# Kernel optimization log

Hardware: AMD Instinct MI355X
Metric: run time of the kernel (lower is better)

## Reference

```python
import jax, jax.numpy as jnp
import numpy as np

EMBED_DIM = 1024
N_HEADS = 16
HEAD_DIM = EMBED_DIM // N_HEADS


def setup_inputs() -> dict:
    key = jax.random.key(0)
    k_x, k_qw, k_qb, k_ow, k_ob = jax.random.split(key, 5)
    s = 1.0 / np.sqrt(EMBED_DIM)
    return {
        "x": jax.random.normal(k_x, (2, 2048, EMBED_DIM), dtype=jnp.float32),
        "qkv_w": jax.random.uniform(k_qw, (3 * EMBED_DIM, EMBED_DIM), jnp.float32, -s, s),
        "qkv_b": jax.random.uniform(k_qb, (3 * EMBED_DIM,), jnp.float32, -s, s),
        "out_w": jax.random.uniform(k_ow, (EMBED_DIM, EMBED_DIM), jnp.float32, -s, s),
        "out_b": jax.random.uniform(k_ob, (EMBED_DIM,), jnp.float32, -s, s),
    }


def reference(x, qkv_w, qkv_b, out_w, out_b):
    B, S, E = x.shape
    # fused QKV projection (torch Linear: x @ W^T + b)
    qkv = x @ qkv_w.T + qkv_b                      # [B,S,3E]
    qkv = qkv.reshape(B, S, N_HEADS, 3 * HEAD_DIM).transpose(0, 2, 1, 3)  # [B,H,S,3d]
    q, k, v = jnp.split(qkv, 3, axis=-1)           # each [B,H,S,d]
    scores = jnp.einsum("bhqd,bhkd->bhqk", q, k) / jnp.sqrt(jnp.float32(HEAD_DIM))
    weights = jax.nn.softmax(scores, axis=-1)      # [B,H,S,S]
    attn = jnp.einsum("bhqk,bhkd->bhqd", weights, v)
    attn = attn.transpose(0, 2, 1, 3).reshape(B, S, E)
    return attn @ out_w.T + out_b
```

## Files before the change

### kernel.cpp

```cpp
#include <hip/hip_runtime.h>
#include <hip/hip_bf16.h>


#define E_DIM   1024
#define NHEADS  16
#define HDIM    64
#define SEQ     2048
#define TOK     4096
#define QKV_DIM 3072
#define QK_STRIDE 2048
#define QSCALE_F 0.18033688011112042f

typedef __attribute__((ext_vector_type(8))) short bf16x8;
typedef __attribute__((ext_vector_type(4))) float f32x4;
typedef __attribute__((ext_vector_type(4))) int   i32x4;
typedef __attribute__((ext_vector_type(2))) int   i32x2;
typedef __attribute__((ext_vector_type(2))) __bf16 bf16x2_t;

__device__ __forceinline__ unsigned short f2bf(float x) {
    union { float f; unsigned u; } a; a.f = x;
    unsigned r = a.u + 0x7FFF + ((a.u >> 16) & 1);
    return (unsigned short)(r >> 16);
}

__device__ __forceinline__ unsigned pack2bf(float a, float b) {
#if __has_builtin(__builtin_amdgcn_cvt_pk_bf16_f32)
    union { bf16x2_t v; unsigned u; } u;
    u.v = __builtin_amdgcn_cvt_pk_bf16_f32(a, b);
    return u.u;
#else
    union { float f; unsigned u; } ua, ub; ua.f = a; ub.f = b;
    unsigned ra = ua.u + 0x7FFF + ((ua.u >> 16) & 1);
    unsigned rb = ub.u + 0x7FFF + ((ub.u >> 16) & 1);
    return (ra >> 16) | (rb & 0xFFFF0000u);
#endif
}

__device__ __forceinline__ void load_lds16(const void* g, void* l) {
    __builtin_amdgcn_global_load_lds(
        (const __attribute__((address_space(1))) void*)g,
        (__attribute__((address_space(3))) void*)l, 16, 0, 0);
}

__device__ __forceinline__ bf16x8 lds_read8(const unsigned short* p) {
    union { i32x4 i; bf16x8 b; } u;
    u.i = *(const i32x4*)p;
    return u.b;
}

__device__ __forceinline__ f32x4 mfma16(bf16x8 a, bf16x8 b, f32x4 c) {
    return __builtin_amdgcn_mfma_f32_16x16x32_bf16(a, b, c, 0, 0, 0);
}

__global__ void cast3_kernel(const float* __restrict__ a, unsigned short* __restrict__ oa, int na4,
                             const float* __restrict__ b, unsigned short* __restrict__ ob, int nb4,
                             const float* __restrict__ c, unsigned short* __restrict__ oc) {
    int i = blockIdx.x * blockDim.x + threadIdx.x;
    const float* src; unsigned short* dst; int j;
    if (i < na4)            { src = a; dst = oa; j = i; }
    else if (i < na4 + nb4) { src = b; dst = ob; j = i - na4; }
    else                    { src = c; dst = oc; j = i - na4 - nb4; }
    f32x4 v = ((const f32x4*)src)[j];
    union { i32x2 i2; unsigned u[2]; } o;
    o.u[0] = pack2bf(v.x, v.y);
    o.u[1] = pack2bf(v.z, v.w);
    ((i32x2*)dst)[j] = o.i2;
}

__global__ __launch_bounds__(256, 3)
void gemm_qkv_kernel(const unsigned short* __restrict__ A,
                     const unsigned short* __restrict__ B,
                     const float* __restrict__ bias,
                     unsigned short* __restrict__ qk,
                     unsigned short* __restrict__ vT,
                     int K) {
    __shared__ __align__(16) unsigned short As[128 * 64];
    __shared__ __align__(16) unsigned short Bs[128 * 64];

    const int tid  = threadIdx.x;
    const int wave = tid >> 6, lane = tid & 63;
    const int quad = lane >> 4, l16 = lane & 15;
    const int row0 = blockIdx.y * 128, col0 = blockIdx.x * 128;
    const int wr = (wave >> 1) * 64, wc = (wave & 1) * 64;

    f32x4 acc[4][4];
#pragma unroll
    for (int i = 0; i < 4; ++i)
#pragma unroll
        for (int j = 0; j < 4; ++j) acc[i][j] = (f32x4){0.f, 0.f, 0.f, 0.f};

    const int nkt = K >> 6;
    for (int kt = 0; kt < nkt; ++kt) {
        const int k0 = kt << 6;
#pragma unroll
        for (int i = 0; i < 4; ++i) {
            int p = i * 256 + tid;
            int r = p >> 3;
            int kc = (p & 7) ^ (r & 7);
            load_lds16(A + (size_t)(row0 + r) * K + k0 + kc * 8, &As[p * 8]);
        }
#pragma unroll
        for (int i = 0; i < 4; ++i) {
            int p = i * 256 + tid;
            int r = p >> 3;
            int kc = (p & 7) ^ (r & 7);
            load_lds16(B + (size_t)(col0 + r) * K + k0 + kc * 8, &Bs[p * 8]);
        }
        __syncthreads();

#pragma unroll
        for (int ks = 0; ks < 2; ++ks) {
            bf16x8 af[4], bfr[4];
#pragma unroll
            for (int rb = 0; rb < 4; ++rb) {
                int r_l  = wr + rb * 16 + l16;
                int phys = (ks * 4 + quad) ^ (l16 & 7);
                af[rb] = lds_read8(&As[r_l * 64 + phys * 8]);
            }
#pragma unroll
            for (int cb = 0; cb < 4; ++cb) {
                int r_l  = wc + cb * 16 + l16;
                int phys = (ks * 4 + quad) ^ (l16 & 7);
                bfr[cb] = lds_read8(&Bs[r_l * 64 + phys * 8]);
            }
#pragma unroll
            for (int rb = 0; rb < 4; ++rb)
#pragma unroll
                for (int cb = 0; cb < 4; ++cb)
                    acc[rb][cb] = mfma16(af[rb], bfr[cb], acc[rb][cb]);
        }
        __syncthreads();
    }

#pragma unroll
    for (int rb = 0; rb < 4; ++rb)
#pragma unroll
        for (int cb = 0; cb < 4; ++cb) {
            int col = col0 + wc + cb * 16 + l16;
            int h    = col / 192;
            int part = col - h * 192;
            float bv = bias[col];
            int row_b = row0 + wr + rb * 16 + quad * 4;
            float v[4];
#pragma unroll
            for (int reg = 0; reg < 4; ++reg) v[reg] = acc[rb][cb][reg] + bv;
            if (part < 128) {
                float sc = (part < 64) ? QSCALE_F : 1.0f;
                size_t base = (size_t)h * 128 + part;
#pragma unroll
                for (int reg = 0; reg < 4; ++reg)
                    qk[(size_t)(row_b + reg) * QK_STRIDE + base] = f2bf(v[reg] * sc);
            } else {
                int i  = part - 128;
                int b  = row_b >> 11;
                int s  = row_b & 2047;
                i32x2 pk;
                pk.x = (int)pack2bf(v[0], v[1]);
                pk.y = (int)pack2bf(v[2], v[3]);
                *(i32x2*)&vT[(((size_t)(b * 16 + h)) * 64 + i) * SEQ + s] = pk;
            }
        }
}

__global__ __launch_bounds__(256, 2)
void gemm2_kernel(const unsigned short* __restrict__ A,
                  const unsigned short* __restrict__ B,
                  const float* __restrict__ bias,
                  float* __restrict__ C, int M, int N, int K) {
    __shared__ __align__(16) unsigned short As[128 * 64];
    __shared__ __align__(16) unsigned short Bs[64 * 64];

    const int tid  = threadIdx.x;
    const int wave = tid >> 6, lane = tid & 63;
    const int quad = lane >> 4, l16 = lane & 15;
    const int row0 = blockIdx.y * 128, col0 = blockIdx.x * 64;
    const int wr = wave * 32;

    f32x4 acc[2][4];
#pragma unroll
    for (int i = 0; i < 2; ++i)
#pragma unroll
        for (int j = 0; j < 4; ++j) acc[i][j] = (f32x4){0.f, 0.f, 0.f, 0.f};

    const int nkt = K >> 6;
    for (int kt = 0; kt < nkt; ++kt) {
        const int k0 = kt << 6;
#pragma unroll
        for (int i = 0; i < 4; ++i) {
            int p = i * 256 + tid;
            int r = p >> 3;
            int kc = (p & 7) ^ (r & 7);
            load_lds16(A + (size_t)(row0 + r) * K + k0 + kc * 8, &As[p * 8]);
        }
#pragma unroll
        for (int i = 0; i < 2; ++i) {
            int p = i * 256 + tid;
            int r = p >> 3;
            int kc = (p & 7) ^ (r & 7);
            load_lds16(B + (size_t)(col0 + r) * K + k0 + kc * 8, &Bs[p * 8]);
        }
        __syncthreads();

#pragma unroll
        for (int ks = 0; ks < 2; ++ks) {
            bf16x8 af[2], bfr[4];
#pragma unroll
            for (int rb = 0; rb < 2; ++rb) {
                int r_l  = wr + rb * 16 + l16;
                int phys = (ks * 4 + quad) ^ (l16 & 7);
                af[rb] = lds_read8(&As[r_l * 64 + phys * 8]);
            }
#pragma unroll
            for (int cb = 0; cb < 4; ++cb) {
                int r_l  = cb * 16 + l16;
                int phys = (ks * 4 + quad) ^ (l16 & 7);
                bfr[cb] = lds_read8(&Bs[r_l * 64 + phys * 8]);
            }
#pragma unroll
            for (int rb = 0; rb < 2; ++rb)
#pragma unroll
                for (int cb = 0; cb < 4; ++cb)
                    acc[rb][cb] = mfma16(af[rb], bfr[cb], acc[rb][cb]);
        }
        __syncthreads();
    }

#pragma unroll
    for (int rb = 0; rb < 2; ++rb)
#pragma unroll
        for (int cb = 0; cb < 4; ++cb) {
            int col = col0 + cb * 16 + l16;
            float bv = bias[col];
#pragma unroll
            for (int reg = 0; reg < 4; ++reg) {
                int row = row0 + wr + rb * 16 + quad * 4 + reg;
                C[(size_t)row * N + col] = acc[rb][cb][reg] + bv;
            }
        }
}

__global__ __launch_bounds__(256, 4)
void attn_kernel(const unsigned short* __restrict__ qk,
                 const unsigned short* __restrict__ vT,
                 unsigned short* __restrict__ attn) {
    __shared__ __align__(16) unsigned short Ks[128 * 64];
    __shared__ __align__(16) unsigned short Vs[64 * 128];
    __shared__ __align__(16) unsigned short Ps[4][16 * 64];

    const int tid  = threadIdx.x;
    const int wave = tid >> 6, lane = tid & 63;
    const int quad = lane >> 4, l16 = lane & 15;
    const int bh = blockIdx.y;
    const int b = bh >> 4, h = bh & 15;
    const int q0 = blockIdx.x * 64;
    const size_t rowbase = (size_t)b * SEQ;
    const int qtok = q0 + wave * 16 + l16;

    bf16x8 qf[2];
#pragma unroll
    for (int ks = 0; ks < 2; ++ks) {
        const unsigned short* p =
            qk + (rowbase + qtok) * QK_STRIDE + h * 128 + ks * 32 + quad * 8;
        union { i32x4 i; bf16x8 b; } u;
        u.i = *(const i32x4*)p;
        qf[ks] = u.b;
    }

    f32x4 o[4];
#pragma unroll
    for (int ib = 0; ib < 4; ++ib) o[ib] = (f32x4){0.f, 0.f, 0.f, 0.f};
    float l_s = 0.f;

    for (int kt = 0; kt < SEQ / 128; ++kt) {
        const int kb = kt * 128;
        const unsigned short* kbase = qk + (rowbase + kb) * QK_STRIDE + h * 128 + 64;
        const unsigned short* vbase = vT + (size_t)bh * 64 * SEQ + kb;
#pragma unroll
        for (int i = 0; i < 4; ++i) {
            int p = i * 256 + tid;
            int r = p >> 3;
            int kc = (p & 7) ^ (r & 7);
            load_lds16(kbase + r * QK_STRIDE + kc * 8, &Ks[p * 8]);
        }
#pragma unroll
        for (int i = 0; i < 4; ++i) {
            int p = i * 256 + tid;
            int r = p >> 4;
            int c = (p & 15) ^ (r & 15);
            load_lds16(vbase + r * SEQ + c * 8, &Vs[p * 8]);
        }
        __syncthreads();

        f32x4 s[8];
#pragma unroll
        for (int cb = 0; cb < 8; ++cb) s[cb] = (f32x4){0.f, 0.f, 0.f, 0.f};
#pragma unroll
        for (int ks = 0; ks < 2; ++ks)
#pragma unroll
            for (int cb = 0; cb < 8; ++cb) {
                int phys = (ks * 4 + quad) ^ (l16 & 7);
                bf16x8 kf = lds_read8(&Ks[(cb * 16 + l16) * 64 + phys * 8]);
                s[cb] = mfma16(kf, qf[ks], s[cb]);
            }

        float rs = 0.f;
#pragma unroll
        for (int cb = 0; cb < 8; ++cb)
#pragma unroll
            for (int r = 0; r < 4; ++r) {
                float pv = exp2f(s[cb][r]);
                s[cb][r] = pv;
                rs += pv;
            }
        rs += __shfl_xor(rs, 16);
        rs += __shfl_xor(rs, 32);
        l_s += rs;

#pragma unroll
        for (int half = 0; half < 2; ++half) {
#pragma unroll
            for (int c4 = 0; c4 < 4; ++c4) {
                int cb = half * 4 + c4;
                i32x2 pk;
                pk.x = (int)pack2bf(s[cb][0], s[cb][1]);
                pk.y = (int)pack2bf(s[cb][2], s[cb][3]);
                int off = l16 * 64 + (((c4 * 2 + (quad >> 1)) ^ (l16 & 7)) * 8)
                        + (quad & 1) * 4;
                *(i32x2*)&Ps[wave][off] = pk;
            }
            __asm__ volatile("s_waitcnt lgkmcnt(0)" ::: "memory");
#pragma unroll
            for (int kc2 = 0; kc2 < 2; ++kc2) {
                bf16x8 pf = lds_read8(
                    &Ps[wave][l16 * 64 + (((kc2 * 4 + quad) ^ (l16 & 7)) * 8)]);
#pragma unroll
                for (int ib = 0; ib < 4; ++ib) {
                    int hk = half * 2 + kc2;
                    int phys = (hk * 4 + quad) ^ l16;
                    bf16x8 vf = lds_read8(&Vs[(ib * 16 + l16) * 128 + phys * 8]);
                    o[ib] = mfma16(pf, vf, o[ib]);
                }
            }
        }
        __syncthreads();
    }

    float il[4];
#pragma unroll
    for (int r = 0; r < 4; ++r) il[r] = 1.0f / __shfl(l_s, quad * 4 + r);
#pragma unroll
    for (int ib = 0; ib < 4; ++ib)
#pragma unroll
        for (int r = 0; r < 4; ++r) {
            int t = q0 + wave * 16 + quad * 4 + r;
            attn[(rowbase + t) * E_DIM + h * 64 + ib * 16 + l16] =
                f2bf(o[ib][r] * il[r]);
        }
}

extern "C" void kernel_launch(void* const* d_in, const int* in_sizes, int n_in,
                              void* d_out, int out_size, void* d_ws, size_t ws_size,
                              hipStream_t stream) {
    const float* x     = (const float*)d_in[0];
    const float* qkv_w = (const float*)d_in[1];
    const float* qkv_b = (const float*)d_in[2];
    const float* out_w = (const float*)d_in[3];
    const float* out_b = (const float*)d_in[4];

    char* ws = (char*)d_ws;
    unsigned short* xb   = (unsigned short*)(ws);
    unsigned short* wqkv = (unsigned short*)(ws + 8388608);
    unsigned short* wout = (unsigned short*)(ws + 14680064);
    unsigned short* qk   = (unsigned short*)(ws + 16777216);
    unsigned short* attn = (unsigned short*)(ws + 33554432);
    unsigned short* vT   = (unsigned short*)(ws + 41943040);

    cast3_kernel<<<8192, 256, 0, stream>>>(x, xb, 1048576,
                                           qkv_w, wqkv, 786432,
                                           out_w, wout);

    gemm_qkv_kernel<<<dim3(24, 32), 256, 0, stream>>>(
        xb, wqkv, qkv_b, qk, vT, E_DIM);

    attn_kernel<<<dim3(32, 32), 256, 0, stream>>>(qk, vT, attn);

    gemm2_kernel<<<dim3(16, 32), 256, 0, stream>>>(
        attn, wout, out_b, (float*)d_out, TOK, E_DIM, E_DIM);
}
```

Measured before the change: 207.7 us.

## Double attention block to 128 queries with 8 waves sharing K/V tiles

The attention kernel now runs 512 threads per block covering 128 query rows, so each K/V tile staged in LDS serves twice as many queries and the total global K/V traffic is halved. LDS addresses are precomputed as per-lane base pointers to cut index arithmetic inside the loop. exp2f is swapped for the hardware exp2 builtin, and f2bf now uses the packed conversion. The risks are fewer blocks in the grid (512 instead of 1024) and higher register pressure under the new launch bounds.

```diff
diff --git a/kernel.cpp b/kernel.cpp
--- a/kernel.cpp
+++ b/kernel.cpp
@@ -17,11 +17,11 @@
 typedef __attribute__((ext_vector_type(2))) int   i32x2;
 typedef __attribute__((ext_vector_type(2))) __bf16 bf16x2_t;
 
-__device__ __forceinline__ unsigned short f2bf(float x) {
-    union { float f; unsigned u; } a; a.f = x;
-    unsigned r = a.u + 0x7FFF + ((a.u >> 16) & 1);
-    return (unsigned short)(r >> 16);
-}
+#if __has_builtin(__builtin_amdgcn_exp2f)
+#define EXP2F(x) __builtin_amdgcn_exp2f(x)
+#else
+#define EXP2F(x) exp2f(x)
+#endif
 
 __device__ __forceinline__ unsigned pack2bf(float a, float b) {
 #if __has_builtin(__builtin_amdgcn_cvt_pk_bf16_f32)
@@ -34,6 +34,10 @@
     unsigned rb = ub.u + 0x7FFF + ((ub.u >> 16) & 1);
     return (ra >> 16) | (rb & 0xFFFF0000u);
 #endif
+}
+
+__device__ __forceinline__ unsigned short f2bf(float x) {
+    return (unsigned short)(pack2bf(x, x) & 0xFFFFu);
 }
 
 __device__ __forceinline__ void load_lds16(const void* g, void* l) {
@@ -239,22 +243,37 @@
         }
 }
 
-__global__ __launch_bounds__(256, 4)
+__global__ __launch_bounds__(512, 4)
 void attn_kernel(const unsigned short* __restrict__ qk,
                  const unsigned short* __restrict__ vT,
                  unsigned short* __restrict__ attn) {
     __shared__ __align__(16) unsigned short Ks[128 * 64];
     __shared__ __align__(16) unsigned short Vs[64 * 128];
-    __shared__ __align__(16) unsigned short Ps[4][16 * 64];
+    __shared__ __align__(16) unsigned short Ps[8][16 * 64];
 
     const int tid  = threadIdx.x;
     const int wave = tid >> 6, lane = tid & 63;
     const int quad = lane >> 4, l16 = lane & 15;
     const int bh = blockIdx.y;
     const int b = bh >> 4, h = bh & 15;
-    const int q0 = blockIdx.x * 64;
+    const int q0 = blockIdx.x * 128;
     const size_t rowbase = (size_t)b * SEQ;
     const int qtok = q0 + wave * 16 + l16;
+
+    const int sw3 = l16 & 7;
+    const unsigned short* Kb0 = &Ks[l16 * 64 + ((quad ^ sw3) * 8)];
+    const unsigned short* Kb1 = &Ks[l16 * 64 + (((4 + quad) ^ sw3) * 8)];
+    const unsigned short* Vb[4] = {
+        &Vs[l16 * 128 + (((0 * 4 + quad) ^ l16) * 8)],
+        &Vs[l16 * 128 + (((1 * 4 + quad) ^ l16) * 8)],
+        &Vs[l16 * 128 + (((2 * 4 + quad) ^ l16) * 8)],
+        &Vs[l16 * 128 + (((3 * 4 + quad) ^ l16) * 8)] };
+    unsigned short* Pw[4];
+#pragma unroll
+    for (int c4 = 0; c4 < 4; ++c4)
+        Pw[c4] = &Ps[wave][l16 * 64 + (((c4 * 2 + (quad >> 1)) ^ sw3) * 8) + (quad & 1) * 4];
+    const unsigned short* Pr0 = &Ps[wave][l16 * 64 + ((quad ^ sw3) * 8)];
+    const unsigned short* Pr1 = &Ps[wave][l16 * 64 + (((4 + quad) ^ sw3) * 8)];
 
     bf16x8 qf[2];
 #pragma unroll
@@ -276,15 +295,15 @@
         const unsigned short* kbase = qk + (rowbase + kb) * QK_STRIDE + h * 128 + 64;
         const unsigned short* vbase = vT + (size_t)bh * 64 * SEQ + kb;
 #pragma unroll
-        for (int i = 0; i < 4; ++i) {
-            int p = i * 256 + tid;
+        for (int i = 0; i < 2; ++i) {
+            int p = i * 512 + tid;
             int r = p >> 3;
             int kc = (p & 7) ^ (r & 7);
             load_lds16(kbase + r * QK_STRIDE + kc * 8, &Ks[p * 8]);
         }
 #pragma unroll
-        for (int i = 0; i < 4; ++i) {
-            int p = i * 256 + tid;
+        for (int i = 0; i < 2; ++i) {
+            int p = i * 512 + tid;
             int r = p >> 4;
             int c = (p & 15) ^ (r & 15);
             load_lds16(vbase + r * SEQ + c * 8, &Vs[p * 8]);
@@ -295,20 +314,22 @@
 #pragma unroll
         for (int cb = 0; cb < 8; ++cb) s[cb] = (f32x4){0.f, 0.f, 0.f, 0.f};
 #pragma unroll
-        for (int ks = 0; ks < 2; ++ks)
-#pragma unroll
-            for (int cb = 0; cb < 8; ++cb) {
-                int phys = (ks * 4 + quad) ^ (l16 & 7);
-                bf16x8 kf = lds_read8(&Ks[(cb * 16 + l16) * 64 + phys * 8]);
-                s[cb] = mfma16(kf, qf[ks], s[cb]);
-            }
+        for (int cb = 0; cb < 8; ++cb) {
+            bf16x8 kf0 = lds_read8(Kb0 + cb * 1024);
+            s[cb] = mfma16(kf0, qf[0], s[cb]);
+        }
+#pragma unroll
+        for (int cb = 0; cb < 8; ++cb) {
+            bf16x8 kf1 = lds_read8(Kb1 + cb * 1024);
+            s[cb] = mfma16(kf1, qf[1], s[cb]);
+        }
 
         float rs = 0.f;
 #pragma unroll
         for (int cb = 0; cb < 8; ++cb)
 #pragma unroll
             for (int r = 0; r < 4; ++r) {
-                float pv = exp2f(s[cb][r]);
+                float pv = EXP2F(s[cb][r]);
                 s[cb][r] = pv;
                 rs += pv;
             }
@@ -324,21 +345,21 @@
                 i32x2 pk;
                 pk.x = (int)pack2bf(s[cb][0], s[cb][1]);
                 pk.y = (int)pack2bf(s[cb][2], s[cb][3]);
-                int off = l16 * 64 + (((c4 * 2 + (quad >> 1)) ^ (l16 & 7)) * 8)
-                        + (quad & 1) * 4;
-                *(i32x2*)&Ps[wave][off] = pk;
+                *(i32x2*)Pw[c4] = pk;
             }
             __asm__ volatile("s_waitcnt lgkmcnt(0)" ::: "memory");
-#pragma unroll
-            for (int kc2 = 0; kc2 < 2; ++kc2) {
-                bf16x8 pf = lds_read8(
-                    &Ps[wave][l16 * 64 + (((kc2 * 4 + quad) ^ (l16 & 7)) * 8)]);
+            {
+                bf16x8 pf0 = lds_read8(Pr0);
 #pragma unroll
                 for (int ib = 0; ib < 4; ++ib) {
-                    int hk = half * 2 + kc2;
-                    int phys = (hk * 4 + quad) ^ l16;
-                    bf16x8 vf = lds_read8(&Vs[(ib * 16 + l16) * 128 + phys * 8]);
-                    o[ib] = mfma16(pf, vf, o[ib]);
+                    bf16x8 vf = lds_read8(Vb[half * 2 + 0] + ib * 2048);
+                    o[ib] = mfma16(pf0, vf, o[ib]);
+                }
+                bf16x8 pf1 = lds_read8(Pr1);
+#pragma unroll
+                for (int ib = 0; ib < 4; ++ib) {
+                    bf16x8 vf = lds_read8(Vb[half * 2 + 1] + ib * 2048);
+                    o[ib] = mfma16(pf1, vf, o[ib]);
                 }
             }
         }
@@ -382,7 +403,7 @@
     gemm_qkv_kernel<<<dim3(24, 32), 256, 0, stream>>>(
         xb, wqkv, qkv_b, qk, vT, E_DIM);
 
-    attn_kernel<<<dim3(32, 32), 256, 0, stream>>>(qk, vT, attn);
+    attn_kernel<<<dim3(16, 32), 512, 0, stream>>>(qk, vT, attn);
 
     gemm2_kernel<<<dim3(16, 32), 256, 0, stream>>>(
         attn, wout, out_b, (float*)d_out, TOK, E_DIM, E_DIM);
```

After: 184.1 us. 11.4% less time.
